# Kernel tuning notes

Hardware: AMD Instinct MI355X
Metric: run time of the kernel (lower is better)

The kernel has to match this reference:

```python
import jax, jax.numpy as jnp
import numpy as np

N = 200000  # nodes
C = 256     # per-node feature dim

def setup_inputs() -> dict:
    key = jax.random.key(0)
    k1, k2, k3, k4, k5, k6, k7 = jax.random.split(key, 7)
    out1 = jax.random.normal(k1, (N, C), dtype=jnp.float32)
    out2 = jax.random.normal(k2, (N, C), dtype=jnp.float32)
    neighbour = jax.random.randint(k3, (N, 3), 0, N, dtype=jnp.int64)
    # Combination2: Conv1d(512,512,1) == Linear(512->512)
    W_comb = jax.random.normal(k4, (512, 2 * C), dtype=jnp.float32) * (1.0 / np.sqrt(2 * C))
    b_comb = jax.random.normal(k5, (512,), dtype=jnp.float32) * 0.01
    # Aggregation2: Conv1d(256,512,1) == Linear(256->512)
    W_agg = jax.random.normal(k6, (512, C), dtype=jnp.float32) * (1.0 / np.sqrt(C))
    b_agg = jax.random.normal(k7, (512,), dtype=jnp.float32) * 0.01
    return {"out1": out1, "out2": out2, "neighbour": neighbour,
            "W_comb": W_comb, "b_comb": b_comb, "W_agg": W_agg, "b_agg": b_agg}


def reference(out1, out2, neighbour, W_comb, b_comb, W_agg, b_agg):
    # Combination2: concat features then 1x1 conv (per-node linear)
    a1 = jnp.concatenate([out1, out2], axis=1)              # [N, 512]
    out3 = jnp.einsum('nc,oc->no', a1, W_comb) + b_comb     # [N, 512]

    # Aggregation2: mean of self + 3 gathered neighbors, then linear 256->512
    neigh_feats = jnp.take(out2, neighbour, axis=0)          # [N, 3, C]
    agg = (out2 + neigh_feats.sum(axis=1)) * 0.25            # [N, C]
    out4 = jnp.einsum('nc,oc->no', agg, W_agg) + b_agg       # [N, 512]
    return (out3, out4)
```

## Files before the change

### kernel.cpp

```cpp
#include <hip/hip_runtime.h>


typedef __bf16 bf16x8 __attribute__((ext_vector_type(8)));
typedef float f32x4 __attribute__((ext_vector_type(4)));

#define N_NODES 200000
#define BM 32
#define ROWC 520
#define ROWA 264

__device__ __forceinline__ unsigned short f2bf(float x) {
  union { float f; unsigned int u; } v; v.f = x;
  return (unsigned short)((v.u + 0x7FFFu + ((v.u >> 16) & 1u)) >> 16);
}

__device__ __forceinline__ void st_bf4(unsigned short* p, float4 f) {
  uint2 w;
  w.x = (unsigned int)f2bf(f.x) | ((unsigned int)f2bf(f.y) << 16);
  w.y = (unsigned int)f2bf(f.z) | ((unsigned int)f2bf(f.w) << 16);
  *reinterpret_cast<uint2*>(p) = w;
}

__global__ void pack_w_kernel(const float* __restrict__ Wc,
                              const float* __restrict__ Wa,
                              unsigned short* __restrict__ Pc,
                              unsigned short* __restrict__ Pa) {
  int t = blockIdx.x * 256 + threadIdx.x;
  if (t >= (512 + 256) * 64) return;
  int lane = t & 63;
  int tile = t >> 6;
  const float* W;
  unsigned short* P;
  int K, kt_n;
  if (tile < 512) { W = Wc; P = Pc; K = 512; kt_n = 16; }
  else { tile -= 512; W = Wa; P = Pa; K = 256; kt_n = 8; }
  int nt = tile / kt_n;
  int kt = tile - nt * kt_n;
  int row = nt * 16 + (lane & 15);
  int k0 = kt * 32 + (lane >> 4) * 8;
  const float* src = W + (size_t)row * K + k0;
  unsigned short* dst = P + (size_t)tile * 512 + lane * 8;
#pragma unroll
  for (int j = 0; j < 8; ++j) dst[j] = f2bf(src[j]);
}

__global__ __launch_bounds__(512, 4) void mesh_fused_kernel(
    const float* __restrict__ out1,
    const float* __restrict__ out2,
    const int* __restrict__ nbr,
    const unsigned short* __restrict__ Pc,
    const unsigned short* __restrict__ Pa,
    const float* __restrict__ b_comb,
    const float* __restrict__ b_agg,
    float* __restrict__ outp) {
  __shared__ unsigned short Acomb[BM * ROWC];
  __shared__ unsigned short Aagg[BM * ROWA];

  const int tid = threadIdx.x;
  const long long node0 = (long long)blockIdx.x * BM;

  {
    const int ln = tid >> 4;
    const int c16 = tid & 15;
    const long long gn = node0 + ln;
    const long long nb = gn * 3;
    long long i0 = nbr[nb + 0];
    long long i1 = nbr[nb + 1];
    long long i2 = nbr[nb + 2];
    i0 = i0 < 0 ? 0 : (i0 >= N_NODES ? N_NODES - 1 : i0);
    i1 = i1 < 0 ? 0 : (i1 >= N_NODES ? N_NODES - 1 : i1);
    i2 = i2 < 0 ? 0 : (i2 >= N_NODES ? N_NODES - 1 : i2);
    const float4* r1 = reinterpret_cast<const float4*>(out1 + gn * 256);
    const float4* r2 = reinterpret_cast<const float4*>(out2 + gn * 256);
    const float4* g0 = reinterpret_cast<const float4*>(out2 + i0 * 256);
    const float4* g1 = reinterpret_cast<const float4*>(out2 + i1 * 256);
    const float4* g2 = reinterpret_cast<const float4*>(out2 + i2 * 256);
#pragma unroll
    for (int r = 0; r < 4; ++r) {
      const int c = c16 + 16 * r;
      float4 f1 = r1[c];
      float4 f2 = r2[c];
      float4 n0 = g0[c];
      float4 n1 = g1[c];
      float4 n2 = g2[c];
      float4 ag;
      ag.x = (f2.x + n0.x + n1.x + n2.x) * 0.25f;
      ag.y = (f2.y + n0.y + n1.y + n2.y) * 0.25f;
      ag.z = (f2.z + n0.z + n1.z + n2.z) * 0.25f;
      ag.w = (f2.w + n0.w + n1.w + n2.w) * 0.25f;
      st_bf4(&Acomb[ln * ROWC + c * 4], f1);
      st_bf4(&Acomb[ln * ROWC + 256 + c * 4], f2);
      st_bf4(&Aagg[ln * ROWA + c * 4], ag);
    }
  }
  __syncthreads();

  const int wave = tid >> 6;
  const int lane = tid & 63;
  const int l15 = lane & 15;
  const int l4 = lane >> 4;

  f32x4 acc3[2][4], acc4[2][4];
#pragma unroll
  for (int m = 0; m < 2; ++m)
#pragma unroll
    for (int n = 0; n < 4; ++n) {
      acc3[m][n] = (f32x4){0.f, 0.f, 0.f, 0.f};
      acc4[m][n] = (f32x4){0.f, 0.f, 0.f, 0.f};
    }

  const int nt0 = wave * 4;

  {
    const unsigned short* pc = Pc + (size_t)nt0 * 16 * 512 + lane * 8;
    const unsigned short* a_base = &Acomb[(size_t)l15 * ROWC + l4 * 8];
#pragma unroll
    for (int kt = 0; kt < 16; ++kt) {
      bf16x8 a0 = *reinterpret_cast<const bf16x8*>(a_base + kt * 32);
      bf16x8 a1 = *reinterpret_cast<const bf16x8*>(a_base + 16 * ROWC + kt * 32);
#pragma unroll
      for (int n = 0; n < 4; ++n) {
        bf16x8 b = *reinterpret_cast<const bf16x8*>(pc + ((size_t)n * 16 + kt) * 512);
        acc3[0][n] = __builtin_amdgcn_mfma_f32_16x16x32_bf16(a0, b, acc3[0][n], 0, 0, 0);
        acc3[1][n] = __builtin_amdgcn_mfma_f32_16x16x32_bf16(a1, b, acc3[1][n], 0, 0, 0);
      }
    }
  }

  {
    const unsigned short* pa = Pa + (size_t)nt0 * 8 * 512 + lane * 8;
    const unsigned short* a_base = &Aagg[(size_t)l15 * ROWA + l4 * 8];
#pragma unroll
    for (int kt = 0; kt < 8; ++kt) {
      bf16x8 a0 = *reinterpret_cast<const bf16x8*>(a_base + kt * 32);
      bf16x8 a1 = *reinterpret_cast<const bf16x8*>(a_base + 16 * ROWA + kt * 32);
#pragma unroll
      for (int n = 0; n < 4; ++n) {
        bf16x8 b = *reinterpret_cast<const bf16x8*>(pa + ((size_t)n * 8 + kt) * 512);
        acc4[0][n] = __builtin_amdgcn_mfma_f32_16x16x32_bf16(a0, b, acc4[0][n], 0, 0, 0);
        acc4[1][n] = __builtin_amdgcn_mfma_f32_16x16x32_bf16(a1, b, acc4[1][n], 0, 0, 0);
      }
    }
  }

  float* o3 = outp;
  float* o4 = outp + (size_t)N_NODES * 512;
#pragma unroll
  for (int n = 0; n < 4; ++n) {
    const int col = wave * 64 + n * 16 + l15;
    const float bc = b_comb[col];
    const float ba = b_agg[col];
#pragma unroll
    for (int m = 0; m < 2; ++m) {
#pragma unroll
      for (int r = 0; r < 4; ++r) {
        const long long row = node0 + m * 16 + l4 * 4 + r;
        o3[row * 512 + col] = acc3[m][n][r] + bc;
        o4[row * 512 + col] = acc4[m][n][r] + ba;
      }
    }
  }
}

extern "C" void kernel_launch(void* const* d_in, const int* in_sizes, int n_in,
                              void* d_out, int out_size, void* d_ws, size_t ws_size,
                              hipStream_t stream) {
  const float* out1 = (const float*)d_in[0];
  const float* out2 = (const float*)d_in[1];
  const int* nbr = (const int*)d_in[2];
  const float* Wc = (const float*)d_in[3];
  const float* bc = (const float*)d_in[4];
  const float* Wa = (const float*)d_in[5];
  const float* ba = (const float*)d_in[6];

  unsigned short* Pc = (unsigned short*)d_ws;
  unsigned short* Pa = Pc + 512 * 512;

  pack_w_kernel<<<192, 256, 0, stream>>>(Wc, Wa, Pc, Pa);
  mesh_fused_kernel<<<N_NODES / BM, 512, 0, stream>>>(out1, out2, nbr, Pc, Pa, bc, ba,
                                                      (float*)d_out);
}
```

Baseline: 573.8 us.

## Process multiple node tiles per block with software-prefetched gathers

Each block now handles three 32-node tiles in a loop. While the MFMA GEMM for the current tile runs, it prefetches the next tile's input rows and neighbour gathers into registers, and the neighbour indices two tiles ahead. Bias loads are hoisted out of the tile loop, and launch_bounds no longer requests four blocks per CU. The aim is to hide global load latency behind compute, at the cost of many more live registers and about three times fewer blocks, which may reduce occupancy and parallelism.

```diff
diff --git a/kernel.cpp b/kernel.cpp
--- a/kernel.cpp
+++ b/kernel.cpp
@@ -6,6 +6,8 @@
 
 #define N_NODES 200000
 #define BM 32
+#define NTILES (N_NODES / BM)
+#define TPB 3
 #define ROWC 520
 #define ROWA 264
 
@@ -44,7 +46,7 @@
   for (int j = 0; j < 8; ++j) dst[j] = f2bf(src[j]);
 }
 
-__global__ __launch_bounds__(512, 4) void mesh_fused_kernel(
+__global__ __launch_bounds__(512) void mesh_fused_kernel(
     const float* __restrict__ out1,
     const float* __restrict__ out2,
     const int* __restrict__ nbr,
@@ -57,106 +59,139 @@
   __shared__ unsigned short Aagg[BM * ROWA];
 
   const int tid = threadIdx.x;
-  const long long node0 = (long long)blockIdx.x * BM;
-
-  {
-    const int ln = tid >> 4;
-    const int c16 = tid & 15;
-    const long long gn = node0 + ln;
-    const long long nb = gn * 3;
-    long long i0 = nbr[nb + 0];
-    long long i1 = nbr[nb + 1];
-    long long i2 = nbr[nb + 2];
-    i0 = i0 < 0 ? 0 : (i0 >= N_NODES ? N_NODES - 1 : i0);
-    i1 = i1 < 0 ? 0 : (i1 >= N_NODES ? N_NODES - 1 : i1);
-    i2 = i2 < 0 ? 0 : (i2 >= N_NODES ? N_NODES - 1 : i2);
+  const int ln = tid >> 4;
+  const int c16 = tid & 15;
+  const int wave = tid >> 6, lane = tid & 63;
+  const int l15 = lane & 15, l4 = lane >> 4;
+
+  const int t0 = blockIdx.x * TPB;
+  const int tEnd = (t0 + TPB < NTILES) ? t0 + TPB : NTILES;
+
+  float bcv[4], bav[4];
+#pragma unroll
+  for (int n = 0; n < 4; ++n) {
+    const int col = wave * 64 + n * 16 + l15;
+    bcv[n] = b_comb[col];
+    bav[n] = b_agg[col];
+  }
+
+  float4 s1[4], s2[4], g0v[4], g1v[4], g2v[4];
+  int j0 = 0, j1 = 0, j2 = 0;
+
+  auto load_idx = [&](int t, int& a, int& b, int& c) {
+    const int gn = t * BM + ln;
+    a = nbr[3 * gn + 0];
+    b = nbr[3 * gn + 1];
+    c = nbr[3 * gn + 2];
+  };
+  auto issue_loads = [&](int t, int a, int b, int c) {
+    a = a < 0 ? 0 : (a >= N_NODES ? N_NODES - 1 : a);
+    b = b < 0 ? 0 : (b >= N_NODES ? N_NODES - 1 : b);
+    c = c < 0 ? 0 : (c >= N_NODES ? N_NODES - 1 : c);
+    const size_t gn = (size_t)t * BM + ln;
     const float4* r1 = reinterpret_cast<const float4*>(out1 + gn * 256);
     const float4* r2 = reinterpret_cast<const float4*>(out2 + gn * 256);
-    const float4* g0 = reinterpret_cast<const float4*>(out2 + i0 * 256);
-    const float4* g1 = reinterpret_cast<const float4*>(out2 + i1 * 256);
-    const float4* g2 = reinterpret_cast<const float4*>(out2 + i2 * 256);
+    const float4* g0 = reinterpret_cast<const float4*>(out2 + (size_t)a * 256);
+    const float4* g1 = reinterpret_cast<const float4*>(out2 + (size_t)b * 256);
+    const float4* g2 = reinterpret_cast<const float4*>(out2 + (size_t)c * 256);
 #pragma unroll
     for (int r = 0; r < 4; ++r) {
-      const int c = c16 + 16 * r;
-      float4 f1 = r1[c];
-      float4 f2 = r2[c];
-      float4 n0 = g0[c];
-      float4 n1 = g1[c];
-      float4 n2 = g2[c];
+      const int cc = c16 + 16 * r;
+      s1[r] = r1[cc];
+      s2[r] = r2[cc];
+      g0v[r] = g0[cc];
+      g1v[r] = g1[cc];
+      g2v[r] = g2[cc];
+    }
+  };
+
+  {
+    int a, b, c;
+    load_idx(t0, a, b, c);
+    issue_loads(t0, a, b, c);
+    if (t0 + 1 < tEnd) load_idx(t0 + 1, j0, j1, j2);
+  }
+
+  for (int t = t0; t < tEnd; ++t) {
+    __builtin_amdgcn_s_barrier();
+
+#pragma unroll
+    for (int r = 0; r < 4; ++r) {
+      const int cc = c16 + 16 * r;
       float4 ag;
-      ag.x = (f2.x + n0.x + n1.x + n2.x) * 0.25f;
-      ag.y = (f2.y + n0.y + n1.y + n2.y) * 0.25f;
-      ag.z = (f2.z + n0.z + n1.z + n2.z) * 0.25f;
-      ag.w = (f2.w + n0.w + n1.w + n2.w) * 0.25f;
-      st_bf4(&Acomb[ln * ROWC + c * 4], f1);
-      st_bf4(&Acomb[ln * ROWC + 256 + c * 4], f2);
-      st_bf4(&Aagg[ln * ROWA + c * 4], ag);
-    }
-  }
-  __syncthreads();
-
-  const int wave = tid >> 6;
-  const int lane = tid & 63;
-  const int l15 = lane & 15;
-  const int l4 = lane >> 4;
-
-  f32x4 acc3[2][4], acc4[2][4];
-#pragma unroll
-  for (int m = 0; m < 2; ++m)
-#pragma unroll
-    for (int n = 0; n < 4; ++n) {
-      acc3[m][n] = (f32x4){0.f, 0.f, 0.f, 0.f};
-      acc4[m][n] = (f32x4){0.f, 0.f, 0.f, 0.f};
-    }
-
-  const int nt0 = wave * 4;
-
-  {
-    const unsigned short* pc = Pc + (size_t)nt0 * 16 * 512 + lane * 8;
-    const unsigned short* a_base = &Acomb[(size_t)l15 * ROWC + l4 * 8];
-#pragma unroll
-    for (int kt = 0; kt < 16; ++kt) {
-      bf16x8 a0 = *reinterpret_cast<const bf16x8*>(a_base + kt * 32);
-      bf16x8 a1 = *reinterpret_cast<const bf16x8*>(a_base + 16 * ROWC + kt * 32);
+      ag.x = (s2[r].x + g0v[r].x + g1v[r].x + g2v[r].x) * 0.25f;
+      ag.y = (s2[r].y + g0v[r].y + g1v[r].y + g2v[r].y) * 0.25f;
+      ag.z = (s2[r].z + g0v[r].z + g1v[r].z + g2v[r].z) * 0.25f;
+      ag.w = (s2[r].w + g0v[r].w + g1v[r].w + g2v[r].w) * 0.25f;
+      st_bf4(&Acomb[ln * ROWC + cc * 4], s1[r]);
+      st_bf4(&Acomb[ln * ROWC + 256 + cc * 4], s2[r]);
+      st_bf4(&Aagg[ln * ROWA + cc * 4], ag);
+    }
+
+    if (t + 1 < tEnd) {
+      issue_loads(t + 1, j0, j1, j2);
+      if (t + 2 < tEnd) load_idx(t + 2, j0, j1, j2);
+    }
+
+    asm volatile("s_waitcnt lgkmcnt(0)" ::: "memory");
+    __builtin_amdgcn_s_barrier();
+
+    f32x4 acc3[2][4], acc4[2][4];
+#pragma unroll
+    for (int m = 0; m < 2; ++m)
 #pragma unroll
       for (int n = 0; n < 4; ++n) {
-        bf16x8 b = *reinterpret_cast<const bf16x8*>(pc + ((size_t)n * 16 + kt) * 512);
-        acc3[0][n] = __builtin_amdgcn_mfma_f32_16x16x32_bf16(a0, b, acc3[0][n], 0, 0, 0);
-        acc3[1][n] = __builtin_amdgcn_mfma_f32_16x16x32_bf16(a1, b, acc3[1][n], 0, 0, 0);
-      }
-    }
-  }
-
-  {
-    const unsigned short* pa = Pa + (size_t)nt0 * 8 * 512 + lane * 8;
-    const unsigned short* a_base = &Aagg[(size_t)l15 * ROWA + l4 * 8];
-#pragma unroll
-    for (int kt = 0; kt < 8; ++kt) {
-      bf16x8 a0 = *reinterpret_cast<const bf16x8*>(a_base + kt * 32);
-      bf16x8 a1 = *reinterpret_cast<const bf16x8*>(a_base + 16 * ROWA + kt * 32);
-#pragma unroll
-      for (int n = 0; n < 4; ++n) {
-        bf16x8 b = *reinterpret_cast<const bf16x8*>(pa + ((size_t)n * 8 + kt) * 512);
-        acc4[0][n] = __builtin_amdgcn_mfma_f32_16x16x32_bf16(a0, b, acc4[0][n], 0, 0, 0);
-        acc4[1][n] = __builtin_amdgcn_mfma_f32_16x16x32_bf16(a1, b, acc4[1][n], 0, 0, 0);
-      }
-    }
-  }
-
-  float* o3 = outp;
-  float* o4 = outp + (size_t)N_NODES * 512;
-#pragma unroll
-  for (int n = 0; n < 4; ++n) {
-    const int col = wave * 64 + n * 16 + l15;
-    const float bc = b_comb[col];
-    const float ba = b_agg[col];
+        acc3[m][n] = (f32x4){0.f, 0.f, 0.f, 0.f};
+        acc4[m][n] = (f32x4){0.f, 0.f, 0.f, 0.f};
+      }
+
+    const int nt0 = wave * 4;
+    {
+      const unsigned short* pc = Pc + (size_t)nt0 * 16 * 512 + lane * 8;
+      const unsigned short* a_base = &Acomb[(size_t)l15 * ROWC + l4 * 8];
+#pragma unroll
+      for (int kt = 0; kt < 16; ++kt) {
+        bf16x8 a0 = *reinterpret_cast<const bf16x8*>(a_base + kt * 32);
+        bf16x8 a1 = *reinterpret_cast<const bf16x8*>(a_base + 16 * ROWC + kt * 32);
+#pragma unroll
+        for (int n = 0; n < 4; ++n) {
+          bf16x8 b = *reinterpret_cast<const bf16x8*>(pc + ((size_t)n * 16 + kt) * 512);
+          acc3[0][n] = __builtin_amdgcn_mfma_f32_16x16x32_bf16(a0, b, acc3[0][n], 0, 0, 0);
+          acc3[1][n] = __builtin_amdgcn_mfma_f32_16x16x32_bf16(a1, b, acc3[1][n], 0, 0, 0);
+        }
+      }
+    }
+    {
+      const unsigned short* pa = Pa + (size_t)nt0 * 8 * 512 + lane * 8;
+      const unsigned short* a_base = &Aagg[(size_t)l15 * ROWA + l4 * 8];
+#pragma unroll
+      for (int kt = 0; kt < 8; ++kt) {
+        bf16x8 a0 = *reinterpret_cast<const bf16x8*>(a_base + kt * 32);
+        bf16x8 a1 = *reinterpret_cast<const bf16x8*>(a_base + 16 * ROWA + kt * 32);
+#pragma unroll
+        for (int n = 0; n < 4; ++n) {
+          bf16x8 b = *reinterpret_cast<const bf16x8*>(pa + ((size_t)n * 8 + kt) * 512);
+          acc4[0][n] = __builtin_amdgcn_mfma_f32_16x16x32_bf16(a0, b, acc4[0][n], 0, 0, 0);
+          acc4[1][n] = __builtin_amdgcn_mfma_f32_16x16x32_bf16(a1, b, acc4[1][n], 0, 0, 0);
+        }
+      }
+    }
+
+    const long long node0 = (long long)t * BM;
+    float* const o3base = outp + (long long)(node0)*512 + wave * 64 + l15;
+    float* const o4base = o3base + (long long)N_NODES * 512;
 #pragma unroll
     for (int m = 0; m < 2; ++m) {
 #pragma unroll
       for (int r = 0; r < 4; ++r) {
-        const long long row = node0 + m * 16 + l4 * 4 + r;
-        o3[row * 512 + col] = acc3[m][n][r] + bc;
-        o4[row * 512 + col] = acc4[m][n][r] + ba;
+        const long long roff = (long long)(m * 16 + l4 * 4 + r) * 512;
+        float* p3 = o3base + roff;
+        float* p4 = o4base + roff;
+#pragma unroll
+        for (int n = 0; n < 4; ++n) {
+          p3[n * 16] = acc3[m][n][r] + bcv[n];
+          p4[n * 16] = acc4[m][n][r] + bav[n];
+        }
       }
     }
   }
@@ -177,6 +212,7 @@
   unsigned short* Pa = Pc + 512 * 512;
 
   pack_w_kernel<<<192, 256, 0, stream>>>(Wc, Wa, Pc, Pa);
-  mesh_fused_kernel<<<N_NODES / BM, 512, 0, stream>>>(out1, out2, nbr, Pc, Pa, bc, ba,
-                                                      (float*)d_out);
-}
+  const int grid = (NTILES + TPB - 1) / TPB;
+  mesh_fused_kernel<<<grid, 512, 0, stream>>>(out1, out2, nbr, Pc, Pa, bc, ba,
+                                              (float*)d_out);
+}
```

Result: slower. 1.111 ms (+93.7%).

## Reorder aggregation as linear-then-gather via bf16 intermediate, persistent prefetching GEMM

Applied to the files above, without the earlier changes.

Uses linearity to compute Y = out2·W_aggᵀ first and then average the gathered rows of Y, instead of gathering 256-wide fp32 rows and then multiplying. The GEMM kernel becomes persistent with register prefetch of the next tile and nontemporal stores. A separate gather kernel reads bf16 Y rows (1 KB each) for self plus three neighbours and adds the bias. This removes the random fp32 gather from the GEMM path and drops its MFMA work, but writes and rereads a 200 MB bf16 intermediate and rounds the result to bf16 before averaging. It needs a large workspace and falls back to the old fused kernel when the workspace is too small.

```diff
diff --git a/kernel.cpp b/kernel.cpp
--- a/kernel.cpp
+++ b/kernel.cpp
@@ -6,8 +6,11 @@
 
 #define N_NODES 200000
 #define BM 32
+#define NTILES (N_NODES / BM)
 #define ROWC 520
 #define ROWA 264
+#define GRID_A 512
+#define GRID_B 2048
 
 __device__ __forceinline__ unsigned short f2bf(float x) {
   union { float f; unsigned int u; } v; v.f = x;
@@ -44,29 +47,187 @@
   for (int j = 0; j < 8; ++j) dst[j] = f2bf(src[j]);
 }
 
-__global__ __launch_bounds__(512, 4) void mesh_fused_kernel(
-    const float* __restrict__ out1,
-    const float* __restrict__ out2,
+__global__ __launch_bounds__(512, 4) void gemm_kernel(
+    const float* __restrict__ out1, const float* __restrict__ out2,
+    const unsigned short* __restrict__ Pc, const unsigned short* __restrict__ Pa,
+    const float* __restrict__ b_comb,
+    float* __restrict__ out3, unsigned short* __restrict__ Y) {
+  __shared__ unsigned short Acomb[BM * ROWC];
+
+  const int tid = threadIdx.x;
+  const int ln = tid >> 4, c16 = tid & 15;
+  const int wave = tid >> 6, lane = tid & 63;
+  const int l15 = lane & 15, l4 = lane >> 4;
+
+  float bcv[4];
+#pragma unroll
+  for (int n = 0; n < 4; ++n) bcv[n] = b_comb[wave * 64 + n * 16 + l15];
+
+  float4 s1[4], s2[4];
+  auto issue = [&](int t) {
+    const size_t gn = (size_t)t * BM + ln;
+    const float4* r1 = reinterpret_cast<const float4*>(out1 + gn * 256);
+    const float4* r2 = reinterpret_cast<const float4*>(out2 + gn * 256);
+#pragma unroll
+    for (int r = 0; r < 4; ++r) {
+      s1[r] = r1[c16 + 16 * r];
+      s2[r] = r2[c16 + 16 * r];
+    }
+  };
+
+  int t = blockIdx.x;
+  issue(t);
+  while (t < NTILES) {
+    __builtin_amdgcn_s_barrier();
+
+#pragma unroll
+    for (int r = 0; r < 4; ++r) {
+      const int cc = c16 + 16 * r;
+      st_bf4(&Acomb[ln * ROWC + cc * 4], s1[r]);
+      st_bf4(&Acomb[ln * ROWC + 256 + cc * 4], s2[r]);
+    }
+
+    const int tn = t + GRID_A;
+    if (tn < NTILES) issue(tn);
+
+    asm volatile("s_waitcnt lgkmcnt(0)" ::: "memory");
+    __builtin_amdgcn_s_barrier();
+
+    const int nt0 = wave * 4;
+    const long long node0 = (long long)t * BM;
+
+    {
+      f32x4 acc[2][4];
+#pragma unroll
+      for (int m = 0; m < 2; ++m)
+#pragma unroll
+        for (int n = 0; n < 4; ++n) acc[m][n] = (f32x4){0.f, 0.f, 0.f, 0.f};
+
+      const unsigned short* pc = Pc + (size_t)nt0 * 16 * 512 + lane * 8;
+      const unsigned short* ab = &Acomb[(size_t)l15 * ROWC + l4 * 8];
+#pragma unroll
+      for (int kt = 0; kt < 16; ++kt) {
+        bf16x8 a0 = *reinterpret_cast<const bf16x8*>(ab + kt * 32);
+        bf16x8 a1 = *reinterpret_cast<const bf16x8*>(ab + 16 * ROWC + kt * 32);
+#pragma unroll
+        for (int n = 0; n < 4; ++n) {
+          bf16x8 b = *reinterpret_cast<const bf16x8*>(pc + ((size_t)n * 16 + kt) * 512);
+          acc[0][n] = __builtin_amdgcn_mfma_f32_16x16x32_bf16(a0, b, acc[0][n], 0, 0, 0);
+          acc[1][n] = __builtin_amdgcn_mfma_f32_16x16x32_bf16(a1, b, acc[1][n], 0, 0, 0);
+        }
+      }
+      float* o3 = out3 + node0 * 512 + wave * 64 + l15;
+#pragma unroll
+      for (int m = 0; m < 2; ++m)
+#pragma unroll
+        for (int r = 0; r < 4; ++r) {
+          float* p = o3 + (long long)(m * 16 + l4 * 4 + r) * 512;
+#pragma unroll
+          for (int n = 0; n < 4; ++n)
+            __builtin_nontemporal_store(acc[m][n][r] + bcv[n], p + n * 16);
+        }
+    }
+
+    {
+      f32x4 acc[2][4];
+#pragma unroll
+      for (int m = 0; m < 2; ++m)
+#pragma unroll
+        for (int n = 0; n < 4; ++n) acc[m][n] = (f32x4){0.f, 0.f, 0.f, 0.f};
+
+      const unsigned short* pa = Pa + (size_t)nt0 * 8 * 512 + lane * 8;
+      const unsigned short* ab = &Acomb[(size_t)l15 * ROWC + 256 + l4 * 8];
+#pragma unroll
+      for (int kt = 0; kt < 8; ++kt) {
+        bf16x8 a0 = *reinterpret_cast<const bf16x8*>(ab + kt * 32);
+        bf16x8 a1 = *reinterpret_cast<const bf16x8*>(ab + 16 * ROWC + kt * 32);
+#pragma unroll
+        for (int n = 0; n < 4; ++n) {
+          bf16x8 b = *reinterpret_cast<const bf16x8*>(pa + ((size_t)n * 8 + kt) * 512);
+          acc[0][n] = __builtin_amdgcn_mfma_f32_16x16x32_bf16(a0, b, acc[0][n], 0, 0, 0);
+          acc[1][n] = __builtin_amdgcn_mfma_f32_16x16x32_bf16(a1, b, acc[1][n], 0, 0, 0);
+        }
+      }
+      unsigned short* yb = Y + node0 * 512 + wave * 64 + l15;
+#pragma unroll
+      for (int m = 0; m < 2; ++m)
+#pragma unroll
+        for (int r = 0; r < 4; ++r) {
+          unsigned short* p = yb + (long long)(m * 16 + l4 * 4 + r) * 512;
+#pragma unroll
+          for (int n = 0; n < 4; ++n) p[n * 16] = f2bf(acc[m][n][r]);
+        }
+    }
+    t = tn;
+  }
+}
+
+__device__ __forceinline__ float bf_lo(unsigned u) {
+  union { unsigned x; float f; } c; c.x = u << 16; return c.f;
+}
+__device__ __forceinline__ float bf_hi(unsigned u) {
+  union { unsigned x; float f; } c; c.x = u & 0xFFFF0000u; return c.f;
+}
+
+__global__ __launch_bounds__(256) void gather_kernel(
+    const unsigned short* __restrict__ Y, const int* __restrict__ nbr,
+    const float* __restrict__ b_agg, float* __restrict__ out4) {
+  const int lane = threadIdx.x & 63;
+  const int wid = (blockIdx.x * 256 + threadIdx.x) >> 6;
+  const int nwaves = (GRID_B * 256) >> 6;
+
+  float ba[8];
+  const float* bp = b_agg + lane * 8;
+#pragma unroll
+  for (int j = 0; j < 8; ++j) ba[j] = bp[j];
+
+  for (int n = wid; n < N_NODES; n += nwaves) {
+    int i0 = nbr[3 * n + 0];
+    int i1 = nbr[3 * n + 1];
+    int i2 = nbr[3 * n + 2];
+    i0 = i0 < 0 ? 0 : (i0 >= N_NODES ? N_NODES - 1 : i0);
+    i1 = i1 < 0 ? 0 : (i1 >= N_NODES ? N_NODES - 1 : i1);
+    i2 = i2 < 0 ? 0 : (i2 >= N_NODES ? N_NODES - 1 : i2);
+
+    const uint4 a  = *reinterpret_cast<const uint4*>(Y + (size_t)n  * 512 + lane * 8);
+    const uint4 b0 = *reinterpret_cast<const uint4*>(Y + (size_t)i0 * 512 + lane * 8);
+    const uint4 b1 = *reinterpret_cast<const uint4*>(Y + (size_t)i1 * 512 + lane * 8);
+    const uint4 b2 = *reinterpret_cast<const uint4*>(Y + (size_t)i2 * 512 + lane * 8);
+
+    const unsigned wa[4] = {a.x, a.y, a.z, a.w};
+    const unsigned w0[4] = {b0.x, b0.y, b0.z, b0.w};
+    const unsigned w1[4] = {b1.x, b1.y, b1.z, b1.w};
+    const unsigned w2[4] = {b2.x, b2.y, b2.z, b2.w};
+    float s[8];
+#pragma unroll
+    for (int w = 0; w < 4; ++w) {
+      s[2 * w]     = bf_lo(wa[w]) + bf_lo(w0[w]) + bf_lo(w1[w]) + bf_lo(w2[w]);
+      s[2 * w + 1] = bf_hi(wa[w]) + bf_hi(w0[w]) + bf_hi(w1[w]) + bf_hi(w2[w]);
+    }
+    f32x4 o0 = {s[0] * 0.25f + ba[0], s[1] * 0.25f + ba[1],
+                s[2] * 0.25f + ba[2], s[3] * 0.25f + ba[3]};
+    f32x4 o1 = {s[4] * 0.25f + ba[4], s[5] * 0.25f + ba[5],
+                s[6] * 0.25f + ba[6], s[7] * 0.25f + ba[7]};
+    f32x4* op = reinterpret_cast<f32x4*>(out4 + (size_t)n * 512 + lane * 8);
+    __builtin_nontemporal_store(o0, op);
+    __builtin_nontemporal_store(o1, op + 1);
+  }
+}
+
+__global__ __launch_bounds__(512, 4) void mesh_fused_fallback(
+    const float* __restrict__ out1, const float* __restrict__ out2,
     const int* __restrict__ nbr,
-    const unsigned short* __restrict__ Pc,
-    const unsigned short* __restrict__ Pa,
-    const float* __restrict__ b_comb,
-    const float* __restrict__ b_agg,
+    const unsigned short* __restrict__ Pc, const unsigned short* __restrict__ Pa,
+    const float* __restrict__ b_comb, const float* __restrict__ b_agg,
     float* __restrict__ outp) {
   __shared__ unsigned short Acomb[BM * ROWC];
   __shared__ unsigned short Aagg[BM * ROWA];
-
   const int tid = threadIdx.x;
   const long long node0 = (long long)blockIdx.x * BM;
-
   {
-    const int ln = tid >> 4;
-    const int c16 = tid & 15;
+    const int ln = tid >> 4, c16 = tid & 15;
     const long long gn = node0 + ln;
-    const long long nb = gn * 3;
-    long long i0 = nbr[nb + 0];
-    long long i1 = nbr[nb + 1];
-    long long i2 = nbr[nb + 2];
+    long long i0 = nbr[3 * gn + 0], i1 = nbr[3 * gn + 1], i2 = nbr[3 * gn + 2];
     i0 = i0 < 0 ? 0 : (i0 >= N_NODES ? N_NODES - 1 : i0);
     i1 = i1 < 0 ? 0 : (i1 >= N_NODES ? N_NODES - 1 : i1);
     i2 = i2 < 0 ? 0 : (i2 >= N_NODES ? N_NODES - 1 : i2);
@@ -78,87 +239,80 @@
 #pragma unroll
     for (int r = 0; r < 4; ++r) {
       const int c = c16 + 16 * r;
-      float4 f1 = r1[c];
-      float4 f2 = r2[c];
-      float4 n0 = g0[c];
-      float4 n1 = g1[c];
-      float4 n2 = g2[c];
+      float4 f1 = r1[c], f2 = r2[c], n0 = g0[c], n1 = g1[c], n2 = g2[c];
       float4 ag;
       ag.x = (f2.x + n0.x + n1.x + n2.x) * 0.25f;
       ag.y = (f2.y + n0.y + n1.y + n2.y) * 0.25f;
       ag.z = (f2.z + n0.z + n1.z + n2.z) * 0.25f;
       ag.w = (f2.w + n0.w + n1.w + n2.w) * 0.25f;
-      st_bf4(&Acomb[ln * ROWC + c * 4], f1);
-      st_bf4(&Acomb[ln * ROWC + 256 + c * 4], f2);
-      st_bf4(&Aagg[ln * ROWA + c * 4], ag);
+      st_bf4(&Acomb[(tid >> 4) * ROWC + c * 4], f1);
+      st_bf4(&Acomb[(tid >> 4) * ROWC + 256 + c * 4], f2);
+      st_bf4(&Aagg[(tid >> 4) * ROWA + c * 4], ag);
     }
   }
   __syncthreads();
-
-  const int wave = tid >> 6;
-  const int lane = tid & 63;
-  const int l15 = lane & 15;
-  const int l4 = lane >> 4;
-
-  f32x4 acc3[2][4], acc4[2][4];
-#pragma unroll
-  for (int m = 0; m < 2; ++m)
-#pragma unroll
-    for (int n = 0; n < 4; ++n) {
-      acc3[m][n] = (f32x4){0.f, 0.f, 0.f, 0.f};
-      acc4[m][n] = (f32x4){0.f, 0.f, 0.f, 0.f};
-    }
-
+  const int wave = tid >> 6, lane = tid & 63;
+  const int l15 = lane & 15, l4 = lane >> 4;
   const int nt0 = wave * 4;
-
+  float* o3 = outp;
+  float* o4 = outp + (size_t)N_NODES * 512;
   {
+    f32x4 acc[2][4];
+#pragma unroll
+    for (int m = 0; m < 2; ++m)
+#pragma unroll
+      for (int n = 0; n < 4; ++n) acc[m][n] = (f32x4){0.f, 0.f, 0.f, 0.f};
     const unsigned short* pc = Pc + (size_t)nt0 * 16 * 512 + lane * 8;
-    const unsigned short* a_base = &Acomb[(size_t)l15 * ROWC + l4 * 8];
+    const unsigned short* ab = &Acomb[(size_t)l15 * ROWC + l4 * 8];
 #pragma unroll
     for (int kt = 0; kt < 16; ++kt) {
-      bf16x8 a0 = *reinterpret_cast<const bf16x8*>(a_base + kt * 32);
-      bf16x8 a1 = *reinterpret_cast<const bf16x8*>(a_base + 16 * ROWC + kt * 32);
+      bf16x8 a0 = *reinterpret_cast<const bf16x8*>(ab + kt * 32);
+      bf16x8 a1 = *reinterpret_cast<const bf16x8*>(ab + 16 * ROWC + kt * 32);
 #pragma unroll
       for (int n = 0; n < 4; ++n) {
         bf16x8 b = *reinterpret_cast<const bf16x8*>(pc + ((size_t)n * 16 + kt) * 512);
-        acc3[0][n] = __builtin_amdgcn_mfma_f32_16x16x32_bf16(a0, b, acc3[0][n], 0, 0, 0);
-        acc3[1][n] = __builtin_amdgcn_mfma_f32_16x16x32_bf16(a1, b, acc3[1][n], 0, 0, 0);
+        acc[0][n] = __builtin_amdgcn_mfma_f32_16x16x32_bf16(a0, b, acc[0][n], 0, 0, 0);
+        acc[1][n] = __builtin_amdgcn_mfma_f32_16x16x32_bf16(a1, b, acc[1][n], 0, 0, 0);
       }
     }
-  }
-
+#pragma unroll
+    for (int m = 0; m < 2; ++m)
+#pragma unroll
+      for (int r = 0; r < 4; ++r)
+#pragma unroll
+        for (int n = 0; n < 4; ++n) {
+          const int col = wave * 64 + n * 16 + l15;
+          o3[(node0 + m * 16 + l4 * 4 + r) * 512 + col] = acc[m][n][r] + b_comb[col];
+        }
+  }
   {
+    f32x4 acc[2][4];
+#pragma unroll
+    for (int m = 0; m < 2; ++m)
+#pragma unroll
+      for (int n = 0; n < 4; ++n) acc[m][n] = (f32x4){0.f, 0.f, 0.f, 0.f};
     const unsigned short* pa = Pa + (size_t)nt0 * 8 * 512 + lane * 8;
-    const unsigned short* a_base = &Aagg[(size_t)l15 * ROWA + l4 * 8];
+    const unsigned short* ab = &Aagg[(size_t)l15 * ROWA + l4 * 8];
 #pragma unroll
     for (int kt = 0; kt < 8; ++kt) {
-      bf16x8 a0 = *reinterpret_cast<const bf16x8*>(a_base + kt * 32);
-      bf16x8 a1 = *reinterpret_cast<const bf16x8*>(a_base + 16 * ROWA + kt * 32);
+      bf16x8 a0 = *reinterpret_cast<const bf16x8*>(ab + kt * 32);
+      bf16x8 a1 = *reinterpret_cast<const bf16x8*>(ab + 16 * ROWA + kt * 32);
 #pragma unroll
       for (int n = 0; n < 4; ++n) {
         bf16x8 b = *reinterpret_cast<const bf16x8*>(pa + ((size_t)n * 8 + kt) * 512);
-        acc4[0][n] = __builtin_amdgcn_mfma_f32_16x16x32_bf16(a0, b, acc4[0][n], 0, 0, 0);
-        acc4[1][n] = __builtin_amdgcn_mfma_f32_16x16x32_bf16(a1, b, acc4[1][n], 0, 0, 0);
+        acc[0][n] = __builtin_amdgcn_mfma_f32_16x16x32_bf16(a0, b, acc[0][n], 0, 0, 0);
+        acc[1][n] = __builtin_amdgcn_mfma_f32_16x16x32_bf16(a1, b, acc[1][n], 0, 0, 0);
       }
     }
-  }
-
-  float* o3 = outp;
-  float* o4 = outp + (size_t)N_NODES * 512;
-#pragma unroll
-  for (int n = 0; n < 4; ++n) {
-    const int col = wave * 64 + n * 16 + l15;
-    const float bc = b_comb[col];
-    const float ba = b_agg[col];
-#pragma unroll
-    for (int m = 0; m < 2; ++m) {
-#pragma unroll
-      for (int r = 0; r < 4; ++r) {
-        const long long row = node0 + m * 16 + l4 * 4 + r;
-        o3[row * 512 + col] = acc3[m][n][r] + bc;
-        o4[row * 512 + col] = acc4[m][n][r] + ba;
-      }
-    }
+#pragma unroll
+    for (int m = 0; m < 2; ++m)
+#pragma unroll
+      for (int r = 0; r < 4; ++r)
+#pragma unroll
+        for (int n = 0; n < 4; ++n) {
+          const int col = wave * 64 + n * 16 + l15;
+          o4[(node0 + m * 16 + l4 * 4 + r) * 512 + col] = acc[m][n][r] + b_agg[col];
+        }
   }
 }
 
@@ -173,10 +327,23 @@
   const float* Wa = (const float*)d_in[5];
   const float* ba = (const float*)d_in[6];
 
-  unsigned short* Pc = (unsigned short*)d_ws;
-  unsigned short* Pa = Pc + 512 * 512;
-
-  pack_w_kernel<<<192, 256, 0, stream>>>(Wc, Wa, Pc, Pa);
-  mesh_fused_kernel<<<N_NODES / BM, 512, 0, stream>>>(out1, out2, nbr, Pc, Pa, bc, ba,
-                                                      (float*)d_out);
-}
+  const size_t yElems = (size_t)N_NODES * 512;
+  const size_t packElems = 512 * 512 + 512 * 256;
+  const size_t need = (yElems + packElems) * 2;
+
+  if (ws_size >= need) {
+    unsigned short* Yw = (unsigned short*)d_ws;
+    unsigned short* Pc = Yw + yElems;
+    unsigned short* Pa = Pc + 512 * 512;
+    pack_w_kernel<<<192, 256, 0, stream>>>(Wc, Wa, Pc, Pa);
+    gemm_kernel<<<GRID_A, 512, 0, stream>>>(out1, out2, Pc, Pa, bc, (float*)d_out, Yw);
+    gather_kernel<<<GRID_B, 256, 0, stream>>>(Yw, nbr, ba,
+                                              (float*)d_out + (size_t)N_NODES * 512);
+  } else {
+    unsigned short* Pc = (unsigned short*)d_ws;
+    unsigned short* Pa = Pc + 512 * 512;
+    pack_w_kernel<<<192, 256, 0, stream>>>(Wc, Wa, Pc, Pa);
+    mesh_fused_fallback<<<NTILES, 512, 0, stream>>>(out1, out2, nbr, Pc, Pa, bc, ba,
+                                                    (float*)d_out);
+  }
+}
```

Result: slower. 1.155 ms (+101.2%).
